# Optimization experiments

Hardware: AMD Instinct MI355X
Metric: run time of the kernel (lower is better)

Reference implementation:

```python
import jax, jax.numpy as jnp
import numpy as np

BN_EPS = 1e-5


def setup_inputs() -> dict:
    key = jax.random.key(0)
    ks = jax.random.split(key, 4)
    B, C, H, W = 4, 256, 64, 64
    Ck, Cv = 64, 256
    x = jax.random.normal(ks[0], (B, C, H, W), dtype=jnp.float32)
    Wk = jax.random.normal(ks[1], (Ck, C), dtype=jnp.float32) * (1.0 / np.sqrt(C))
    bk = jax.random.normal(ks[2], (Ck,), dtype=jnp.float32) * 0.02
    Wv = jax.random.normal(ks[3], (Cv, C), dtype=jnp.float32) * (1.0 / np.sqrt(C))
    bv = jnp.zeros((Cv,), dtype=jnp.float32)
    return {
        "x": x,
        "Wk": Wk,
        "bk": bk,
        "bn_gamma": jnp.ones((Ck,), dtype=jnp.float32),
        "bn_beta": jnp.zeros((Ck,), dtype=jnp.float32),
        "bn_mean": jnp.zeros((Ck,), dtype=jnp.float32),
        "bn_var": jnp.ones((Ck,), dtype=jnp.float32),
        "Wv": Wv,
        "bv": bv,
    }


def reference(x, Wk, bk, bn_gamma, bn_beta, bn_mean, bn_var, Wv, bv):
    B, C, H, W = x.shape
    HW = H * W
    # 1x1 conv == channel matmul; f_query = f_key (shared weights), so Q == K
    k = jnp.einsum("bchw,kc->bkhw", x, Wk) + bk[None, :, None, None]
    # BatchNorm2d (inference mode: running stats)
    inv = bn_gamma * jax.lax.rsqrt(bn_var + BN_EPS)
    k = k * inv[None, :, None, None] + (bn_beta - bn_mean * inv)[None, :, None, None]
    k = k.reshape(B, -1, HW)                      # [B, Ck, HW]
    v = (jnp.einsum("bchw,kc->bkhw", x, Wv) + bv[None, :, None, None]).reshape(B, -1, HW)  # [B, Cv, HW]
    # energy[b,i,j] = sum_c Q[b,c,i] * K[b,c,j]  (no scaling, as in source)
    energy = jnp.einsum("bci,bcj->bij", k, k)     # [B, HW, HW]
    attn = jax.nn.softmax(energy, axis=-1)
    # out[b,c,i] = sum_j V[b,c,j] * attn[i,j]
    out = jnp.einsum("bcj,bij->bci", v, attn)
    return out.reshape(B, -1, H, W)
```

## Files before the change

### kernel.cpp

```cpp
#include <hip/hip_runtime.h>
#include <math.h>

#define BN_EPS 1e-5f

constexpr int B  = 4;
constexpr int C  = 256;
constexpr int HW = 4096;
constexpr int CK = 64;
constexpr int CV = 256;
constexpr int CO = 320;
constexpr int CHG = 2;

typedef short bf16x8 __attribute__((ext_vector_type(8)));
typedef float f32x4  __attribute__((ext_vector_type(4)));

__device__ __forceinline__ ushort f2bf(float f) {
    unsigned u = __float_as_uint(f);
    u += 0x7FFFu + ((u >> 16) & 1u);
    return (ushort)(u >> 16);
}

__device__ __forceinline__ int swzk(int r) {
    return (((r & 3) | ((((r >> 2) ^ (r >> 3)) & 1) << 2)) << 4);
}
__device__ __forceinline__ int swzv(int r) { return (r & 7) << 4; }

__device__ __forceinline__ void gload_lds16(const void* g, void* l) {
    __builtin_amdgcn_global_load_lds(
        (const __attribute__((address_space(1))) unsigned*)g,
        (__attribute__((address_space(3))) unsigned*)l, 16, 0, 0);
}

__global__ __launch_bounds__(256) void wprep(
    const float* __restrict__ Wk, const float* __restrict__ bk,
    const float* __restrict__ gamma, const float* __restrict__ beta,
    const float* __restrict__ mean,  const float* __restrict__ var,
    const float* __restrict__ Wv, const float* __restrict__ bv,
    ushort* __restrict__ Wq, float* __restrict__ bq)
{
    const int co = blockIdx.x;
    const int c  = threadIdx.x;
    float w;
    if (co < CK) {
        float inv = gamma[co] * rsqrtf(var[co] + BN_EPS);
        w = Wk[co * C + c] * inv;
        if (c == 0) bq[co] = bk[co] * inv + (beta[co] - mean[co] * inv);
    } else {
        w = Wv[(co - CK) * C + c];
        if (c == 0) bq[co] = bv[co - CK];
    }
    const int wv  = co / 80, rem = co % 80;
    const int mi  = rem / 16, colw = rem % 16;
    const int ks  = c >> 5, qw = (c >> 3) & 3, e = c & 7;
    Wq[((((((wv * 8 + ks) * 5 + mi) * 4 + qw) * 16 + colw)) << 3) + e] = f2bf(w);
}

__global__ __launch_bounds__(256) void kv_gemm(
    const float* __restrict__ x, const ushort* __restrict__ Wq,
    const float* __restrict__ bq,
    ushort* __restrict__ Kbuf, ushort* __restrict__ Vbuf,
    float* __restrict__ mb, unsigned* __restrict__ Mx)
{
    __shared__ __align__(16) ushort xt[32][C + 8];

    const int t    = threadIdx.x;
    const int lane = t & 63;
    const int wv   = t >> 6;
    const int q    = lane >> 4;
    const int col  = lane & 15;
    const int hw0  = blockIdx.x * 32;
    const int b    = blockIdx.y;

    const float* xb = x + (size_t)b * C * HW;

    {
        const int cq  = (t >> 5) * 4;
        const int hwo = t & 31;
#pragma unroll
        for (int pass = 0; pass < 8; pass++) {
            const int c0 = pass * 32;
            float a0 = xb[(size_t)(c0 + cq + 0) * HW + hw0 + hwo];
            float a1 = xb[(size_t)(c0 + cq + 1) * HW + hw0 + hwo];
            float a2 = xb[(size_t)(c0 + cq + 2) * HW + hw0 + hwo];
            float a3 = xb[(size_t)(c0 + cq + 3) * HW + hw0 + hwo];
            ushort4 u = make_ushort4(f2bf(a0), f2bf(a1), f2bf(a2), f2bf(a3));
            *(ushort4*)&xt[hwo][c0 + cq] = u;
        }
    }
    __syncthreads();

    f32x4 acc[5][2];
#pragma unroll
    for (int mi = 0; mi < 5; mi++)
#pragma unroll
        for (int nt = 0; nt < 2; nt++)
            acc[mi][nt] = (f32x4){0.f, 0.f, 0.f, 0.f};

#pragma unroll
    for (int ks = 0; ks < 8; ks++) {
        bf16x8 av[5], bvv[2];
#pragma unroll
        for (int mi = 0; mi < 5; mi++)
            av[mi] = *(const bf16x8*)(Wq + ((size_t)((wv * 8 + ks) * 5 + mi) << 9) + lane * 8);
#pragma unroll
        for (int nt = 0; nt < 2; nt++)
            bvv[nt] = *(const bf16x8*)&xt[nt * 16 + col][ks * 32 + q * 8];
#pragma unroll
        for (int mi = 0; mi < 5; mi++)
#pragma unroll
            for (int nt = 0; nt < 2; nt++)
                acc[mi][nt] = __builtin_amdgcn_mfma_f32_16x16x32_bf16(av[mi], bvv[nt], acc[mi][nt], 0, 0, 0);
    }

    float ssq[2] = {0.f, 0.f};
#pragma unroll
    for (int mi = 0; mi < 5; mi++) {
        const int cot = wv * 80 + mi * 16;
        float bi[4];
#pragma unroll
        for (int r = 0; r < 4; r++) bi[r] = bq[cot + q * 4 + r];
#pragma unroll
        for (int nt = 0; nt < 2; nt++) {
            const int hw = hw0 + nt * 16 + col;
            float v0 = acc[mi][nt][0] + bi[0];
            float v1 = acc[mi][nt][1] + bi[1];
            float v2 = acc[mi][nt][2] + bi[2];
            float v3 = acc[mi][nt][3] + bi[3];
            if (cot < CK) {
                ushort4 kk = make_ushort4(f2bf(v0), f2bf(v1), f2bf(v2), f2bf(v3));
                *(ushort4*)&Kbuf[((size_t)b * HW + hw) * CK + cot + q * 4] = kk;
                ssq[nt] += v0 * v0 + v1 * v1 + v2 * v2 + v3 * v3;
            } else {
                const int cv = cot - CK + q * 4;
                Vbuf[((size_t)b * CV + cv + 0) * HW + hw] = f2bf(v0);
                Vbuf[((size_t)b * CV + cv + 1) * HW + hw] = f2bf(v1);
                Vbuf[((size_t)b * CV + cv + 2) * HW + hw] = f2bf(v2);
                Vbuf[((size_t)b * CV + cv + 3) * HW + hw] = f2bf(v3);
            }
        }
    }

    if (wv == 0) {
        float mxn = 0.f;
#pragma unroll
        for (int nt = 0; nt < 2; nt++) {
            float ss = ssq[nt];
            ss += __shfl_xor(ss, 16, 64);
            ss += __shfl_xor(ss, 32, 64);
            float nr = sqrtf(ss);
            if (lane < 16) mb[(size_t)b * HW + hw0 + nt * 16 + col] = nr;
            mxn = fmaxf(mxn, nr);
        }
#pragma unroll
        for (int off = 1; off <= 32; off <<= 1)
            mxn = fmaxf(mxn, __shfl_xor(mxn, off, 64));
        if (t == 0) atomicMax(Mx + b, __float_as_uint(mxn));
    }
}

__global__ __launch_bounds__(256, 2) void attn_kernel(
    const ushort* __restrict__ Kbuf, const ushort* __restrict__ Vbuf,
    const float* __restrict__ mb, const unsigned* __restrict__ Mx,
    float* __restrict__ out)
{
    __shared__ __align__(16) ushort Kt[2][64 * 64];
    __shared__ __align__(16) ushort Vt[2][128 * 64];

    const int t    = threadIdx.x;
    const int lane = t & 63;
    const int wv   = t >> 6;
    const int q    = lane >> 4;
    const int col  = lane & 15;

    const unsigned lin = blockIdx.x + 64u * (blockIdx.y + (unsigned)CHG * blockIdx.z);
    const int xcd   = lin & 7;
    const int s_    = lin >> 3;
    const int i0g   = s_ * 64;
    const int chg   = xcd & 1;
    const int b     = xcd >> 1;

    const int iw    = wv * 16 + col;
    const int jperm = (col >> 2) * 8 + (col & 3);

    const ushort* Kb = Kbuf + (size_t)b * HW * CK;
    const ushort* Vb = Vbuf + (size_t)b * CV * HW;
    const int cbase = chg * 128;

    bf16x8 qa[2];
#pragma unroll
    for (int k = 0; k < 2; k++)
        qa[k] = *(const bf16x8*)(Kb + (size_t)(i0g + iw) * CK + k * 32 + q * 8);

    const float Mxf = __uint_as_float(Mx[b]);
    const float m_val = mb[(size_t)b * HW + i0g + iw] * Mxf;

    f32x4 Oacc[8];
#pragma unroll
    for (int mt = 0; mt < 8; mt++)
        Oacc[mt] = (f32x4){0.f, 0.f, 0.f, 0.f};

    float l_acc = 0.f;
    const f32x4 zf = (f32x4){0.f, 0.f, 0.f, 0.f};

#define STAGE(BUF, JN)                                                         \
    {                                                                          \
        const int jn_s = (JN);                                                 \
        _Pragma("unroll")                                                      \
        for (int p = 0; p < 2; p++) {                                          \
            int off = (wv * 2 + p) * 1024 + lane * 16;                         \
            int r = off >> 7, cb = off & 127;                                  \
            const char* g = (const char*)Kb + (size_t)(jn_s + r) * 128         \
                            + (cb ^ swzk(r));                                  \
            gload_lds16(g, (char*)&Kt[BUF][0] + off);                          \
        }                                                                      \
        _Pragma("unroll")                                                      \
        for (int p = 0; p < 4; p++) {                                          \
            int off = (wv * 4 + p) * 1024 + lane * 16;                         \
            int r = off >> 7, cb = off & 127;                                  \
            const char* g = (const char*)Vb                                    \
                            + ((size_t)(cbase + r) * HW + jn_s) * 2            \
                            + (cb ^ swzv(r));                                  \
            gload_lds16(g, (char*)&Vt[BUF][0] + off);                          \
        }                                                                      \
    }

    STAGE(0, 0);
    __syncthreads();

    int cur = 0;
    for (int j0 = 0; j0 < HW; j0 += 64) {
        STAGE(cur ^ 1, (j0 + 64) & (HW - 1));

        const char* KtB = (const char*)&Kt[cur][0];
        const char* VtB = (const char*)&Vt[cur][0];

        f32x4 S[4];
        __builtin_amdgcn_s_setprio(1);
#pragma unroll
        for (int nt = 0; nt < 4; nt++) {
            const int jr = jperm + (nt >> 1) * 32 + (nt & 1) * 4;
            bf16x8 k0 = *(const bf16x8*)(KtB + jr * 128 + ((q * 16) ^ swzk(jr)));
            bf16x8 k1 = *(const bf16x8*)(KtB + jr * 128 + ((64 + q * 16) ^ swzk(jr)));
            S[nt] = __builtin_amdgcn_mfma_f32_16x16x32_bf16(k0, qa[0], zf, 0, 0, 0);
            S[nt] = __builtin_amdgcn_mfma_f32_16x16x32_bf16(k1, qa[1], S[nt], 0, 0, 0);
        }
        __builtin_amdgcn_s_setprio(0);

        bf16x8 w0, w1;
#pragma unroll
        for (int nt = 0; nt < 4; nt++) {
            float p0 = __expf(S[nt][0] - m_val);
            float p1 = __expf(S[nt][1] - m_val);
            float p2 = __expf(S[nt][2] - m_val);
            float p3 = __expf(S[nt][3] - m_val);
            l_acc += (p0 + p1) + (p2 + p3);
            if (nt == 0) {
                w0[0] = (short)f2bf(p0); w0[1] = (short)f2bf(p1);
                w0[2] = (short)f2bf(p2); w0[3] = (short)f2bf(p3);
            } else if (nt == 1) {
                w0[4] = (short)f2bf(p0); w0[5] = (short)f2bf(p1);
                w0[6] = (short)f2bf(p2); w0[7] = (short)f2bf(p3);
            } else if (nt == 2) {
                w1[0] = (short)f2bf(p0); w1[1] = (short)f2bf(p1);
                w1[2] = (short)f2bf(p2); w1[3] = (short)f2bf(p3);
            } else {
                w1[4] = (short)f2bf(p0); w1[5] = (short)f2bf(p1);
                w1[6] = (short)f2bf(p2); w1[7] = (short)f2bf(p3);
            }
        }

        __builtin_amdgcn_s_setprio(1);
#pragma unroll
        for (int mt = 0; mt < 8; mt++) {
            const int vr = mt * 16 + col;
            bf16x8 v0 = *(const bf16x8*)(VtB + vr * 128 + ((q * 16) ^ swzv(vr)));
            bf16x8 v1 = *(const bf16x8*)(VtB + vr * 128 + ((64 + q * 16) ^ swzv(vr)));
            Oacc[mt] = __builtin_amdgcn_mfma_f32_16x16x32_bf16(v0, w0, Oacc[mt], 0, 0, 0);
            Oacc[mt] = __builtin_amdgcn_mfma_f32_16x16x32_bf16(v1, w1, Oacc[mt], 0, 0, 0);
        }
        __builtin_amdgcn_s_setprio(0);

        __syncthreads();
        cur ^= 1;
    }
#undef STAGE

    l_acc += __shfl_xor(l_acc, 16, 64);
    l_acc += __shfl_xor(l_acc, 32, 64);
    const float inv = 1.0f / l_acc;

    float* ob = out + (size_t)b * CV * HW;
#pragma unroll
    for (int mt = 0; mt < 8; mt++)
#pragma unroll
        for (int r = 0; r < 4; r++)
            ob[(size_t)(cbase + mt * 16 + q * 4 + r) * HW + i0g + iw] = Oacc[mt][r] * inv;
}

extern "C" void kernel_launch(void* const* d_in, const int* in_sizes, int n_in,
                              void* d_out, int out_size, void* d_ws, size_t ws_size,
                              hipStream_t stream)
{
    const float* x     = (const float*)d_in[0];
    const float* Wk    = (const float*)d_in[1];
    const float* bk    = (const float*)d_in[2];
    const float* gamma = (const float*)d_in[3];
    const float* beta  = (const float*)d_in[4];
    const float* mean  = (const float*)d_in[5];
    const float* var   = (const float*)d_in[6];
    const float* Wv    = (const float*)d_in[7];
    const float* bv    = (const float*)d_in[8];
    float* out = (float*)d_out;

    ushort*   Kbuf = (ushort*)d_ws;
    ushort*   Vbuf = Kbuf + (size_t)B * HW * CK;
    ushort*   Wq   = Vbuf + (size_t)B * CV * HW;
    float*    bq   = (float*)(Wq + (size_t)CO * C);
    float*    mb   = bq + CO;
    unsigned* Mx   = (unsigned*)(mb + (size_t)B * HW);

    hipMemsetAsync(Mx, 0, B * sizeof(unsigned), stream);

    wprep<<<dim3(CO), 256, 0, stream>>>(Wk, bk, gamma, beta, mean, var, Wv, bv, Wq, bq);

    kv_gemm<<<dim3(HW / 32, B), 256, 0, stream>>>(x, Wq, bq, Kbuf, Vbuf, mb, Mx);

    dim3 g2(HW / 64, CHG, B);
    attn_kernel<<<g2, 256, 0, stream>>>(Kbuf, Vbuf, mb, Mx, out);
}
```

Baseline: 174.6 us.

## Process two query tiles per wave to reuse K/V LDS tiles

Each wave now computes attention for two 16-row query tiles (128 query rows per block), sharing each K and V fragment loaded from LDS across both. The grid is halved and launch bounds drop to one block per CU to accommodate the doubled accumulator registers. This cuts LDS reads and global K/V staging per query, but lowers occupancy and latency hiding.

```diff
diff --git a/kernel.cpp b/kernel.cpp
--- a/kernel.cpp
+++ b/kernel.cpp
@@ -158,7 +158,32 @@
     }
 }
 
-__global__ __launch_bounds__(256, 2) void attn_kernel(
+#define PACKP(S, W0, W1, LACC, MV)                                             \
+    {                                                                          \
+        _Pragma("unroll")                                                      \
+        for (int nt = 0; nt < 4; nt++) {                                       \
+            float p0 = __expf(S[nt][0] - MV);                                  \
+            float p1 = __expf(S[nt][1] - MV);                                  \
+            float p2 = __expf(S[nt][2] - MV);                                  \
+            float p3 = __expf(S[nt][3] - MV);                                  \
+            LACC += (p0 + p1) + (p2 + p3);                                     \
+            if (nt == 0) {                                                     \
+                W0[0] = (short)f2bf(p0); W0[1] = (short)f2bf(p1);              \
+                W0[2] = (short)f2bf(p2); W0[3] = (short)f2bf(p3);              \
+            } else if (nt == 1) {                                              \
+                W0[4] = (short)f2bf(p0); W0[5] = (short)f2bf(p1);              \
+                W0[6] = (short)f2bf(p2); W0[7] = (short)f2bf(p3);              \
+            } else if (nt == 2) {                                              \
+                W1[0] = (short)f2bf(p0); W1[1] = (short)f2bf(p1);              \
+                W1[2] = (short)f2bf(p2); W1[3] = (short)f2bf(p3);              \
+            } else {                                                           \
+                W1[4] = (short)f2bf(p0); W1[5] = (short)f2bf(p1);              \
+                W1[6] = (short)f2bf(p2); W1[7] = (short)f2bf(p3);              \
+            }                                                                  \
+        }                                                                      \
+    }
+
+__global__ __launch_bounds__(256, 1) void attn_kernel(
     const ushort* __restrict__ Kbuf, const ushort* __restrict__ Vbuf,
     const float* __restrict__ mb, const unsigned* __restrict__ Mx,
     float* __restrict__ out)
@@ -172,10 +197,10 @@
     const int q    = lane >> 4;
     const int col  = lane & 15;
 
-    const unsigned lin = blockIdx.x + 64u * (blockIdx.y + (unsigned)CHG * blockIdx.z);
+    const unsigned lin = blockIdx.x + 32u * (blockIdx.y + 2u * blockIdx.z);
     const int xcd   = lin & 7;
     const int s_    = lin >> 3;
-    const int i0g   = s_ * 64;
+    const int i0g   = s_ * 128;
     const int chg   = xcd & 1;
     const int b     = xcd >> 1;
 
@@ -186,20 +211,25 @@
     const ushort* Vb = Vbuf + (size_t)b * CV * HW;
     const int cbase = chg * 128;
 
-    bf16x8 qa[2];
-#pragma unroll
-    for (int k = 0; k < 2; k++)
-        qa[k] = *(const bf16x8*)(Kb + (size_t)(i0g + iw) * CK + k * 32 + q * 8);
+    bf16x8 qaA[2], qaB[2];
+#pragma unroll
+    for (int k = 0; k < 2; k++) {
+        qaA[k] = *(const bf16x8*)(Kb + (size_t)(i0g + iw) * CK + k * 32 + q * 8);
+        qaB[k] = *(const bf16x8*)(Kb + (size_t)(i0g + 64 + iw) * CK + k * 32 + q * 8);
+    }
 
     const float Mxf = __uint_as_float(Mx[b]);
-    const float m_val = mb[(size_t)b * HW + i0g + iw] * Mxf;
-
-    f32x4 Oacc[8];
-#pragma unroll
-    for (int mt = 0; mt < 8; mt++)
-        Oacc[mt] = (f32x4){0.f, 0.f, 0.f, 0.f};
-
-    float l_acc = 0.f;
+    const float mA = mb[(size_t)b * HW + i0g + iw] * Mxf;
+    const float mB = mb[(size_t)b * HW + i0g + 64 + iw] * Mxf;
+
+    f32x4 OA[8], OB[8];
+#pragma unroll
+    for (int mt = 0; mt < 8; mt++) {
+        OA[mt] = (f32x4){0.f, 0.f, 0.f, 0.f};
+        OB[mt] = (f32x4){0.f, 0.f, 0.f, 0.f};
+    }
+
+    float lA = 0.f, lB = 0.f;
     const f32x4 zf = (f32x4){0.f, 0.f, 0.f, 0.f};
 
 #define STAGE(BUF, JN)                                                         \
@@ -234,40 +264,23 @@
         const char* KtB = (const char*)&Kt[cur][0];
         const char* VtB = (const char*)&Vt[cur][0];
 
-        f32x4 S[4];
+        f32x4 SA[4], SB[4];
         __builtin_amdgcn_s_setprio(1);
 #pragma unroll
         for (int nt = 0; nt < 4; nt++) {
             const int jr = jperm + (nt >> 1) * 32 + (nt & 1) * 4;
             bf16x8 k0 = *(const bf16x8*)(KtB + jr * 128 + ((q * 16) ^ swzk(jr)));
             bf16x8 k1 = *(const bf16x8*)(KtB + jr * 128 + ((64 + q * 16) ^ swzk(jr)));
-            S[nt] = __builtin_amdgcn_mfma_f32_16x16x32_bf16(k0, qa[0], zf, 0, 0, 0);
-            S[nt] = __builtin_amdgcn_mfma_f32_16x16x32_bf16(k1, qa[1], S[nt], 0, 0, 0);
+            SA[nt] = __builtin_amdgcn_mfma_f32_16x16x32_bf16(k0, qaA[0], zf, 0, 0, 0);
+            SA[nt] = __builtin_amdgcn_mfma_f32_16x16x32_bf16(k1, qaA[1], SA[nt], 0, 0, 0);
+            SB[nt] = __builtin_amdgcn_mfma_f32_16x16x32_bf16(k0, qaB[0], zf, 0, 0, 0);
+            SB[nt] = __builtin_amdgcn_mfma_f32_16x16x32_bf16(k1, qaB[1], SB[nt], 0, 0, 0);
         }
         __builtin_amdgcn_s_setprio(0);
 
-        bf16x8 w0, w1;
-#pragma unroll
-        for (int nt = 0; nt < 4; nt++) {
-            float p0 = __expf(S[nt][0] - m_val);
-            float p1 = __expf(S[nt][1] - m_val);
-            float p2 = __expf(S[nt][2] - m_val);
-            float p3 = __expf(S[nt][3] - m_val);
-            l_acc += (p0 + p1) + (p2 + p3);
-            if (nt == 0) {
-                w0[0] = (short)f2bf(p0); w0[1] = (short)f2bf(p1);
-                w0[2] = (short)f2bf(p2); w0[3] = (short)f2bf(p3);
-            } else if (nt == 1) {
-                w0[4] = (short)f2bf(p0); w0[5] = (short)f2bf(p1);
-                w0[6] = (short)f2bf(p2); w0[7] = (short)f2bf(p3);
-            } else if (nt == 2) {
-                w1[0] = (short)f2bf(p0); w1[1] = (short)f2bf(p1);
-                w1[2] = (short)f2bf(p2); w1[3] = (short)f2bf(p3);
-            } else {
-                w1[4] = (short)f2bf(p0); w1[5] = (short)f2bf(p1);
-                w1[6] = (short)f2bf(p2); w1[7] = (short)f2bf(p3);
-            }
-        }
+        bf16x8 wA0, wA1, wB0, wB1;
+        PACKP(SA, wA0, wA1, lA, mA);
+        PACKP(SB, wB0, wB1, lB, mB);
 
         __builtin_amdgcn_s_setprio(1);
 #pragma unroll
@@ -275,8 +288,10 @@
             const int vr = mt * 16 + col;
             bf16x8 v0 = *(const bf16x8*)(VtB + vr * 128 + ((q * 16) ^ swzv(vr)));
             bf16x8 v1 = *(const bf16x8*)(VtB + vr * 128 + ((64 + q * 16) ^ swzv(vr)));
-            Oacc[mt] = __builtin_amdgcn_mfma_f32_16x16x32_bf16(v0, w0, Oacc[mt], 0, 0, 0);
-            Oacc[mt] = __builtin_amdgcn_mfma_f32_16x16x32_bf16(v1, w1, Oacc[mt], 0, 0, 0);
+            OA[mt] = __builtin_amdgcn_mfma_f32_16x16x32_bf16(v0, wA0, OA[mt], 0, 0, 0);
+            OA[mt] = __builtin_amdgcn_mfma_f32_16x16x32_bf16(v1, wA1, OA[mt], 0, 0, 0);
+            OB[mt] = __builtin_amdgcn_mfma_f32_16x16x32_bf16(v0, wB0, OB[mt], 0, 0, 0);
+            OB[mt] = __builtin_amdgcn_mfma_f32_16x16x32_bf16(v1, wB1, OB[mt], 0, 0, 0);
         }
         __builtin_amdgcn_s_setprio(0);
 
@@ -285,16 +300,22 @@
     }
 #undef STAGE
 
-    l_acc += __shfl_xor(l_acc, 16, 64);
-    l_acc += __shfl_xor(l_acc, 32, 64);
-    const float inv = 1.0f / l_acc;
+    lA += __shfl_xor(lA, 16, 64);
+    lA += __shfl_xor(lA, 32, 64);
+    lB += __shfl_xor(lB, 16, 64);
+    lB += __shfl_xor(lB, 32, 64);
+    const float invA = 1.0f / lA;
+    const float invB = 1.0f / lB;
 
     float* ob = out + (size_t)b * CV * HW;
 #pragma unroll
     for (int mt = 0; mt < 8; mt++)
 #pragma unroll
-        for (int r = 0; r < 4; r++)
-            ob[(size_t)(cbase + mt * 16 + q * 4 + r) * HW + i0g + iw] = Oacc[mt][r] * inv;
+        for (int r = 0; r < 4; r++) {
+            const size_t c = cbase + mt * 16 + q * 4 + r;
+            ob[c * HW + i0g + iw]      = OA[mt][r] * invA;
+            ob[c * HW + i0g + 64 + iw] = OB[mt][r] * invB;
+        }
 }
 
 extern "C" void kernel_launch(void* const* d_in, const int* in_sizes, int n_in,
@@ -325,6 +346,6 @@
 
     kv_gemm<<<dim3(HW / 32, B), 256, 0, stream>>>(x, Wq, bq, Kbuf, Vbuf, mb, Mx);
 
-    dim3 g2(HW / 64, CHG, B);
+    dim3 g2(HW / 128, CHG, B);
     attn_kernel<<<g2, 256, 0, stream>>>(Kbuf, Vbuf, mb, Mx, out);
 }
```

New measurement: 197.5 us. +13.1%, slower.
